# Optimization experiments

Measured on AMD Instinct MI355X. Metric: run time of the kernel, lower is better.

## Reference

```python
import jax, jax.numpy as jnp
import numpy as np

EPS = 1e-5

def _bn(x, g, b):
    # BatchNorm1d in training mode: stats over (batch, length) dims, biased var
    mean = jnp.mean(x, axis=(0, 2), keepdims=True)
    var = jnp.var(x, axis=(0, 2), keepdims=True)
    return (x - mean) * jax.lax.rsqrt(var + EPS) * g[None, :, None] + b[None, :, None]

def _conv1x1(x, w, b):
    # pointwise Conv1d: [B,C,T] x [O,C] -> [B,O,T]
    return jnp.einsum('bct,oc->bot', x, w) + b[None, :, None]

def setup_inputs() -> dict:
    key = jax.random.key(0)
    ks = jax.random.split(key, 4)
    B, C, T = 32, 1024, 2048
    x = jax.random.normal(ks[0], (B, C, T), dtype=jnp.float32)
    w1 = jax.random.normal(ks[1], (256, 1024), dtype=jnp.float32) * (1.0 / np.sqrt(1024))
    w2 = jax.random.normal(ks[2], (64, 256), dtype=jnp.float32) * (1.0 / np.sqrt(256))
    return {
        'x': x,
        'bn1_g': jnp.ones((1024,), jnp.float32), 'bn1_b': jnp.zeros((1024,), jnp.float32),
        'w1': w1, 'b1': jnp.zeros((256,), jnp.float32),
        'bn2_g': jnp.ones((256,), jnp.float32), 'bn2_b': jnp.zeros((256,), jnp.float32),
        'w2': w2, 'b2': jnp.zeros((64,), jnp.float32),
    }

def reference(x, bn1_g, bn1_b, w1, b1, bn2_g, bn2_b, w2, b2):
    # reduction layer: BN -> 1x1 conv -> ReLU (1024 -> 256)
    h = jax.nn.relu(_conv1x1(_bn(x, bn1_g, bn1_b), w1, b1))
    # out layer: BN -> 1x1 conv, no activation (256 -> 64)
    out = _conv1x1(_bn(h, bn2_g, bn2_b), w2, b2)
    o = out.shape[1]
    mu = out[:, : o // 2, :]
    logvar = out[:, o // 2 :, :]
    return (mu, logvar)
```

## Files before the change

kernel.cpp:

```cpp
#include <hip/hip_runtime.h>
#include <hip/hip_bf16.h>

#define B_  32
#define C1  1024
#define C2  256
#define T_  2048
#define EPSF 1e-5f
#define ROWP 40

typedef __attribute__((ext_vector_type(8))) short bf16x8;
typedef __attribute__((ext_vector_type(4))) float f32x4;

static __device__ __forceinline__ unsigned short f2bf(float f) {
    union { float f; unsigned u; } v; v.f = f;
    unsigned r = v.u + 0x7fffu + ((v.u >> 16) & 1u);
    return (unsigned short)(r >> 16);
}
static __device__ __forceinline__ float bf2f(unsigned short h) {
    union { unsigned u; float f; } v; v.u = ((unsigned)h) << 16;
    return v.f;
}

__global__ void k_stats1(const float* __restrict__ x,
                         const float* __restrict__ g1, const float* __restrict__ bb1,
                         float* __restrict__ scale1, float* __restrict__ shift1) {
    int c = blockIdx.x, tid = threadIdx.x;
    float s = 0.f, sq = 0.f;
    for (int b = 0; b < B_; ++b) {
        const float4* row = (const float4*)(x + (size_t)b * C1 * T_ + (size_t)c * T_);
        for (int i = tid; i < T_ / 4; i += 256) {
            float4 v = row[i];
            s  += v.x + v.y + v.z + v.w;
            sq += v.x * v.x + v.y * v.y + v.z * v.z + v.w * v.w;
        }
    }
    __shared__ float rs[256], rq[256];
    rs[tid] = s; rq[tid] = sq; __syncthreads();
    for (int off = 128; off > 0; off >>= 1) {
        if (tid < off) { rs[tid] += rs[tid + off]; rq[tid] += rq[tid + off]; }
        __syncthreads();
    }
    if (tid == 0) {
        float n = (float)(B_ * T_);
        float mean = rs[0] / n;
        float var  = rq[0] / n - mean * mean;
        float sc   = g1[c] * rsqrtf(var + EPSF);
        scale1[c] = sc;
        shift1[c] = bb1[c] - mean * sc;
    }
}

__global__ void k_fold1(const float* __restrict__ w1, const float* __restrict__ b1,
                        const float* __restrict__ scale1, const float* __restrict__ shift1,
                        unsigned short* __restrict__ w1e, float* __restrict__ b1e) {
    int o = blockIdx.x, tid = threadIdx.x;
    float4 w = ((const float4*)(w1 + (size_t)o * C1))[tid];
    int c = tid * 4;
    float p = w.x * shift1[c] + w.y * shift1[c + 1] + w.z * shift1[c + 2] + w.w * shift1[c + 3];
    uint2 pk;
    pk.x = (unsigned)f2bf(w.x * scale1[c])     | ((unsigned)f2bf(w.y * scale1[c + 1]) << 16);
    pk.y = (unsigned)f2bf(w.z * scale1[c + 2]) | ((unsigned)f2bf(w.w * scale1[c + 3]) << 16);
    *((uint2*)(w1e + (size_t)o * C1 + c)) = pk;
    __shared__ float rs[256];
    rs[tid] = p; __syncthreads();
    for (int off = 128; off > 0; off >>= 1) {
        if (tid < off) rs[tid] += rs[tid + off];
        __syncthreads();
    }
    if (tid == 0) b1e[o] = b1[o] + rs[0];
}

__global__ __launch_bounds__(256) void k_gemm1(const float* __restrict__ x,
        const unsigned short* __restrict__ w1e, const float* __restrict__ b1e,
        unsigned short* __restrict__ h) {
    __shared__ unsigned short sA[128 * ROWP];
    __shared__ unsigned short sB[128 * ROWP];
    int bm = blockIdx.x, bn = blockIdx.y, b = blockIdx.z;
    int tid = threadIdx.x;
    int wave = tid >> 6, lane = tid & 63;
    int wm = wave >> 1, wn = wave & 1;
    int l15 = lane & 15, q = lane >> 4;
    f32x4 acc[4][4] = {};
    const size_t xbase = (size_t)b * C1 * T_ + (size_t)bn * 128;

    for (int k0 = 0; k0 < C1; k0 += 32) {
        #pragma unroll
        for (int i = 0; i < 2; ++i) {
            int chunk = tid + i * 256;
            int row = chunk >> 2, cq = chunk & 3;
            uint4 v = *((const uint4*)(w1e + (size_t)(bm * 128 + row) * C1 + k0 + cq * 8));
            *((uint4*)&sA[row * ROWP + cq * 8]) = v;
        }
        #pragma unroll
        for (int i = 0; i < 2; ++i) {
            int task = tid + i * 256;
            int kp = task >> 5, tq = task & 31;
            const float* p0 = x + xbase + (size_t)(k0 + 2 * kp) * T_ + tq * 4;
            float4 r0 = *((const float4*)p0);
            float4 r1 = *((const float4*)(p0 + T_));
            int tl = tq * 4;
            *((unsigned*)&sB[(tl + 0) * ROWP + 2 * kp]) = (unsigned)f2bf(r0.x) | ((unsigned)f2bf(r1.x) << 16);
            *((unsigned*)&sB[(tl + 1) * ROWP + 2 * kp]) = (unsigned)f2bf(r0.y) | ((unsigned)f2bf(r1.y) << 16);
            *((unsigned*)&sB[(tl + 2) * ROWP + 2 * kp]) = (unsigned)f2bf(r0.z) | ((unsigned)f2bf(r1.z) << 16);
            *((unsigned*)&sB[(tl + 3) * ROWP + 2 * kp]) = (unsigned)f2bf(r0.w) | ((unsigned)f2bf(r1.w) << 16);
        }
        __syncthreads();
        bf16x8 af[4], bfr[4];
        #pragma unroll
        for (int mi = 0; mi < 4; ++mi)
            af[mi] = *((const bf16x8*)&sA[(wm * 64 + mi * 16 + l15) * ROWP + q * 8]);
        #pragma unroll
        for (int ni = 0; ni < 4; ++ni)
            bfr[ni] = *((const bf16x8*)&sB[(wn * 64 + ni * 16 + l15) * ROWP + q * 8]);
        #pragma unroll
        for (int mi = 0; mi < 4; ++mi)
            #pragma unroll
            for (int ni = 0; ni < 4; ++ni)
                acc[mi][ni] = __builtin_amdgcn_mfma_f32_16x16x32_bf16(af[mi], bfr[ni], acc[mi][ni], 0, 0, 0);
        __syncthreads();
    }
    int obase = bm * 128 + wm * 64;
    int tbase = bn * 128 + wn * 64;
    #pragma unroll
    for (int mi = 0; mi < 4; ++mi) {
        #pragma unroll
        for (int reg = 0; reg < 4; ++reg) {
            int o = obase + mi * 16 + q * 4 + reg;
            float bias = b1e[o];
            size_t hb = (size_t)b * C2 * T_ + (size_t)o * T_ + tbase;
            #pragma unroll
            for (int ni = 0; ni < 4; ++ni) {
                float v = acc[mi][ni][reg] + bias;
                v = v > 0.f ? v : 0.f;
                h[hb + ni * 16 + l15] = f2bf(v);
            }
        }
    }
}

__global__ void k_stats2(const unsigned short* __restrict__ h,
                         const float* __restrict__ g2, const float* __restrict__ bb2,
                         float* __restrict__ scale2, float* __restrict__ shift2) {
    int c = blockIdx.x, tid = threadIdx.x;
    float s = 0.f, sq = 0.f;
    for (int b = 0; b < B_; ++b) {
        const ushort4* row = (const ushort4*)(h + (size_t)b * C2 * T_ + (size_t)c * T_);
        for (int i = tid; i < T_ / 4; i += 256) {
            ushort4 v = row[i];
            float a0 = bf2f(v.x), a1 = bf2f(v.y), a2 = bf2f(v.z), a3 = bf2f(v.w);
            s  += a0 + a1 + a2 + a3;
            sq += a0 * a0 + a1 * a1 + a2 * a2 + a3 * a3;
        }
    }
    __shared__ float rs[256], rq[256];
    rs[tid] = s; rq[tid] = sq; __syncthreads();
    for (int off = 128; off > 0; off >>= 1) {
        if (tid < off) { rs[tid] += rs[tid + off]; rq[tid] += rq[tid + off]; }
        __syncthreads();
    }
    if (tid == 0) {
        float n = (float)(B_ * T_);
        float mean = rs[0] / n;
        float var  = rq[0] / n - mean * mean;
        float sc   = g2[c] * rsqrtf(var + EPSF);
        scale2[c] = sc;
        shift2[c] = bb2[c] - mean * sc;
    }
}

__global__ void k_fold2(const float* __restrict__ w2, const float* __restrict__ b2,
                        const float* __restrict__ scale2, const float* __restrict__ shift2,
                        unsigned short* __restrict__ w2e, float* __restrict__ b2e) {
    int o = blockIdx.x, tid = threadIdx.x;
    float w = w2[(size_t)o * C2 + tid];
    float p = w * shift2[tid];
    w2e[(size_t)o * C2 + tid] = f2bf(w * scale2[tid]);
    __shared__ float rs[256];
    rs[tid] = p; __syncthreads();
    for (int off = 128; off > 0; off >>= 1) {
        if (tid < off) rs[tid] += rs[tid + off];
        __syncthreads();
    }
    if (tid == 0) b2e[o] = b2[o] + rs[0];
}

__global__ __launch_bounds__(256) void k_gemm2(const unsigned short* __restrict__ h,
        const unsigned short* __restrict__ w2e, const float* __restrict__ b2e,
        float* __restrict__ out) {
    __shared__ unsigned short sA[64 * ROWP];
    __shared__ unsigned short sB[128 * ROWP];
    int bn = blockIdx.x, b = blockIdx.y;
    int tid = threadIdx.x;
    int wave = tid >> 6, lane = tid & 63;
    int l15 = lane & 15, q = lane >> 4;
    f32x4 acc[4][2] = {};
    const size_t hbase = (size_t)b * C2 * T_ + (size_t)bn * 128;

    for (int k0 = 0; k0 < C2; k0 += 32) {
        {
            int row = tid >> 2, cq = tid & 3;
            uint4 v = *((const uint4*)(w2e + (size_t)row * C2 + k0 + cq * 8));
            *((uint4*)&sA[row * ROWP + cq * 8]) = v;
        }
        #pragma unroll
        for (int i = 0; i < 2; ++i) {
            int task = tid + i * 256;
            int kp = task >> 5, tq = task & 31;
            const unsigned short* p0 = h + hbase + (size_t)(k0 + 2 * kp) * T_ + tq * 4;
            uint2 r0 = *((const uint2*)p0);
            uint2 r1 = *((const uint2*)(p0 + T_));
            unsigned a0 = r0.x & 0xffffu, a1 = r0.x >> 16, a2 = r0.y & 0xffffu, a3 = r0.y >> 16;
            unsigned c0 = r1.x & 0xffffu, c1 = r1.x >> 16, c2 = r1.y & 0xffffu, c3 = r1.y >> 16;
            int tl = tq * 4;
            *((unsigned*)&sB[(tl + 0) * ROWP + 2 * kp]) = a0 | (c0 << 16);
            *((unsigned*)&sB[(tl + 1) * ROWP + 2 * kp]) = a1 | (c1 << 16);
            *((unsigned*)&sB[(tl + 2) * ROWP + 2 * kp]) = a2 | (c2 << 16);
            *((unsigned*)&sB[(tl + 3) * ROWP + 2 * kp]) = a3 | (c3 << 16);
        }
        __syncthreads();
        bf16x8 af[4], bfr[2];
        #pragma unroll
        for (int mi = 0; mi < 4; ++mi)
            af[mi] = *((const bf16x8*)&sA[(mi * 16 + l15) * ROWP + q * 8]);
        #pragma unroll
        for (int ni = 0; ni < 2; ++ni)
            bfr[ni] = *((const bf16x8*)&sB[(wave * 32 + ni * 16 + l15) * ROWP + q * 8]);
        #pragma unroll
        for (int mi = 0; mi < 4; ++mi)
            #pragma unroll
            for (int ni = 0; ni < 2; ++ni)
                acc[mi][ni] = __builtin_amdgcn_mfma_f32_16x16x32_bf16(af[mi], bfr[ni], acc[mi][ni], 0, 0, 0);
        __syncthreads();
    }
    int tbase = bn * 128 + wave * 32;
    #pragma unroll
    for (int mi = 0; mi < 4; ++mi) {
        #pragma unroll
        for (int reg = 0; reg < 4; ++reg) {
            int o = mi * 16 + q * 4 + reg;
            float bias = b2e[o];
            size_t base = (o < 32)
                ? ((size_t)b * 32 * T_ + (size_t)o * T_)
                : (2097152u + (size_t)b * 32 * T_ + (size_t)(o - 32) * T_);
            #pragma unroll
            for (int ni = 0; ni < 2; ++ni) {
                int t = tbase + ni * 16 + l15;
                out[base + t] = acc[mi][ni][reg] + bias;
            }
        }
    }
}

extern "C" void kernel_launch(void* const* d_in, const int* in_sizes, int n_in,
                              void* d_out, int out_size, void* d_ws, size_t ws_size,
                              hipStream_t stream) {
    const float* x   = (const float*)d_in[0];
    const float* g1  = (const float*)d_in[1];
    const float* bb1 = (const float*)d_in[2];
    const float* w1  = (const float*)d_in[3];
    const float* b1  = (const float*)d_in[4];
    const float* g2  = (const float*)d_in[5];
    const float* bb2 = (const float*)d_in[6];
    const float* w2  = (const float*)d_in[7];
    const float* b2  = (const float*)d_in[8];
    float* out = (float*)d_out;

    char* ws = (char*)d_ws;
    float* scale1 = (float*)(ws + 0);
    float* shift1 = (float*)(ws + 4096);
    float* b1e    = (float*)(ws + 8192);
    float* scale2 = (float*)(ws + 9216);
    float* shift2 = (float*)(ws + 10240);
    float* b2e    = (float*)(ws + 11264);
    unsigned short* w1e = (unsigned short*)(ws + 12288);
    unsigned short* w2e = (unsigned short*)(ws + 12288 + 524288);
    unsigned short* h   = (unsigned short*)(ws + 573440);

    k_stats1<<<dim3(1024), dim3(256), 0, stream>>>(x, g1, bb1, scale1, shift1);
    k_fold1 <<<dim3(256),  dim3(256), 0, stream>>>(w1, b1, scale1, shift1, w1e, b1e);
    k_gemm1 <<<dim3(2, 16, 32), dim3(256), 0, stream>>>(x, w1e, b1e, h);
    k_stats2<<<dim3(256),  dim3(256), 0, stream>>>(h, g2, bb2, scale2, shift2);
    k_fold2 <<<dim3(64),   dim3(256), 0, stream>>>(w2, b2, scale2, shift2, w2e, b2e);
    k_gemm2 <<<dim3(16, 32), dim3(256), 0, stream>>>(h, w2e, b2e, out);
}
```

Measured before the change: 538.9 us.

## Transpose activations to channel-contiguous bf16 and load GEMM tiles directly to LDS

A new prep kernel reads x once. It computes the BN1 partial sums and also writes a bf16 copy of x transposed to [B,T,C]. Both GEMMs then load K-contiguous tiles with simple 16-byte loads, and GEMM1 uses global_load_lds to copy straight into shared memory. The intermediate h is also stored channel-contiguous, so stats2 becomes a coalesced partial reduction followed by a small finalize kernel. The aim is to avoid re-reading fp32 x for the statistics and to drop the per-element transpose and convert work inside the GEMM loops. In exchange it adds a 128 MB write and read of xT, and the unpadded 32-wide LDS rows may cause bank conflicts.

```diff
diff --git a/kernel.cpp b/kernel.cpp
--- a/kernel.cpp
+++ b/kernel.cpp
@@ -1,12 +1,11 @@
 #include <hip/hip_runtime.h>
-#include <hip/hip_bf16.h>
 
 #define B_  32
 #define C1  1024
 #define C2  256
 #define T_  2048
 #define EPSF 1e-5f
-#define ROWP 40
+#define CPAD 72
 
 typedef __attribute__((ext_vector_type(8))) short bf16x8;
 typedef __attribute__((ext_vector_type(4))) float f32x4;
@@ -20,34 +19,64 @@
     union { unsigned u; float f; } v; v.u = ((unsigned)h) << 16;
     return v.f;
 }
-
-__global__ void k_stats1(const float* __restrict__ x,
-                         const float* __restrict__ g1, const float* __restrict__ bb1,
-                         float* __restrict__ scale1, float* __restrict__ shift1) {
-    int c = blockIdx.x, tid = threadIdx.x;
-    float s = 0.f, sq = 0.f;
-    for (int b = 0; b < B_; ++b) {
-        const float4* row = (const float4*)(x + (size_t)b * C1 * T_ + (size_t)c * T_);
-        for (int i = tid; i < T_ / 4; i += 256) {
-            float4 v = row[i];
+static __device__ __forceinline__ void g2l16(const void* g, void* l) {
+    __builtin_amdgcn_global_load_lds(
+        (const __attribute__((address_space(1))) unsigned int*)g,
+        (__attribute__((address_space(3))) unsigned int*)l, 16, 0, 0);
+}
+
+__global__ __launch_bounds__(256) void k_prep(const float* __restrict__ x,
+        unsigned short* __restrict__ xT, float* __restrict__ psum, float* __restrict__ psq) {
+    __shared__ unsigned short tile[64 * CPAD];
+    __shared__ float red[256];
+    int ct = blockIdx.x, b = blockIdx.y, tid = threadIdx.x;
+    int c0 = ct * 64;
+    int cl = tid >> 2, t4 = tid & 3;
+    const float* xrow = x + (size_t)b * C1 * T_ + (size_t)(c0 + cl) * T_;
+    float s = 0.f, sq = 0.f;
+    for (int t0 = 0; t0 < T_; t0 += 64) {
+        #pragma unroll
+        for (int j = 0; j < 4; ++j) {
+            int tl = j * 16 + t4 * 4;
+            float4 v = *(const float4*)(xrow + t0 + tl);
             s  += v.x + v.y + v.z + v.w;
             sq += v.x * v.x + v.y * v.y + v.z * v.z + v.w * v.w;
-        }
-    }
-    __shared__ float rs[256], rq[256];
-    rs[tid] = s; rq[tid] = sq; __syncthreads();
-    for (int off = 128; off > 0; off >>= 1) {
-        if (tid < off) { rs[tid] += rs[tid + off]; rq[tid] += rq[tid + off]; }
-        __syncthreads();
-    }
-    if (tid == 0) {
-        float n = (float)(B_ * T_);
-        float mean = rs[0] / n;
-        float var  = rq[0] / n - mean * mean;
-        float sc   = g1[c] * rsqrtf(var + EPSF);
-        scale1[c] = sc;
-        shift1[c] = bb1[c] - mean * sc;
-    }
+            tile[(tl + 0) * CPAD + cl] = f2bf(v.x);
+            tile[(tl + 1) * CPAD + cl] = f2bf(v.y);
+            tile[(tl + 2) * CPAD + cl] = f2bf(v.z);
+            tile[(tl + 3) * CPAD + cl] = f2bf(v.w);
+        }
+        __syncthreads();
+        #pragma unroll
+        for (int j = 0; j < 2; ++j) {
+            int w = tid + j * 256;
+            int tl = w >> 3, cu = w & 7;
+            uint4 vv = *(const uint4*)&tile[tl * CPAD + cu * 8];
+            *(uint4*)&xT[((size_t)b * T_ + t0 + tl) * C1 + c0 + cu * 8] = vv;
+        }
+        __syncthreads();
+    }
+    red[tid] = s; __syncthreads();
+    if (tid < 64)
+        psum[(size_t)b * C1 + c0 + tid] = red[4*tid] + red[4*tid+1] + red[4*tid+2] + red[4*tid+3];
+    __syncthreads();
+    red[tid] = sq; __syncthreads();
+    if (tid < 64)
+        psq[(size_t)b * C1 + c0 + tid]  = red[4*tid] + red[4*tid+1] + red[4*tid+2] + red[4*tid+3];
+}
+
+__global__ void k_scales1(const float* __restrict__ psum, const float* __restrict__ psq,
+        const float* __restrict__ g, const float* __restrict__ bb,
+        float* __restrict__ scale, float* __restrict__ shift) {
+    int c = blockIdx.x * 256 + threadIdx.x;
+    float s = 0.f, sq = 0.f;
+    for (int b = 0; b < B_; ++b) { s += psum[b * C1 + c]; sq += psq[b * C1 + c]; }
+    float n = (float)(B_ * T_);
+    float mean = s / n;
+    float var  = sq / n - mean * mean;
+    float sc   = g[c] * rsqrtf(var + EPSF);
+    scale[c] = sc;
+    shift[c] = bb[c] - mean * sc;
 }
 
 __global__ void k_fold1(const float* __restrict__ w1, const float* __restrict__ b1,
@@ -70,48 +99,36 @@
     if (tid == 0) b1e[o] = b1[o] + rs[0];
 }
 
-__global__ __launch_bounds__(256) void k_gemm1(const float* __restrict__ x,
+__global__ __launch_bounds__(256) void k_gemm1(const unsigned short* __restrict__ xT,
         const unsigned short* __restrict__ w1e, const float* __restrict__ b1e,
-        unsigned short* __restrict__ h) {
-    __shared__ unsigned short sA[128 * ROWP];
-    __shared__ unsigned short sB[128 * ROWP];
+        unsigned short* __restrict__ hT) {
+    __shared__ unsigned short sA[128 * 32];
+    __shared__ unsigned short sB[128 * 32];
     int bm = blockIdx.x, bn = blockIdx.y, b = blockIdx.z;
     int tid = threadIdx.x;
     int wave = tid >> 6, lane = tid & 63;
     int wm = wave >> 1, wn = wave & 1;
     int l15 = lane & 15, q = lane >> 4;
     f32x4 acc[4][4] = {};
-    const size_t xbase = (size_t)b * C1 * T_ + (size_t)bn * 128;
+    const unsigned short* xblk = xT + ((size_t)b * T_ + (size_t)bn * 128) * C1;
+    const unsigned short* wblk = w1e + (size_t)(bm * 128) * C1;
 
     for (int k0 = 0; k0 < C1; k0 += 32) {
         #pragma unroll
         for (int i = 0; i < 2; ++i) {
-            int chunk = tid + i * 256;
-            int row = chunk >> 2, cq = chunk & 3;
-            uint4 v = *((const uint4*)(w1e + (size_t)(bm * 128 + row) * C1 + k0 + cq * 8));
-            *((uint4*)&sA[row * ROWP + cq * 8]) = v;
-        }
-        #pragma unroll
-        for (int i = 0; i < 2; ++i) {
-            int task = tid + i * 256;
-            int kp = task >> 5, tq = task & 31;
-            const float* p0 = x + xbase + (size_t)(k0 + 2 * kp) * T_ + tq * 4;
-            float4 r0 = *((const float4*)p0);
-            float4 r1 = *((const float4*)(p0 + T_));
-            int tl = tq * 4;
-            *((unsigned*)&sB[(tl + 0) * ROWP + 2 * kp]) = (unsigned)f2bf(r0.x) | ((unsigned)f2bf(r1.x) << 16);
-            *((unsigned*)&sB[(tl + 1) * ROWP + 2 * kp]) = (unsigned)f2bf(r0.y) | ((unsigned)f2bf(r1.y) << 16);
-            *((unsigned*)&sB[(tl + 2) * ROWP + 2 * kp]) = (unsigned)f2bf(r0.z) | ((unsigned)f2bf(r1.z) << 16);
-            *((unsigned*)&sB[(tl + 3) * ROWP + 2 * kp]) = (unsigned)f2bf(r0.w) | ((unsigned)f2bf(r1.w) << 16);
+            int idx = (wave * 2 + i) * 64 + lane;
+            int row = idx >> 2, cq = idx & 3;
+            g2l16(wblk + (size_t)row * C1 + k0 + cq * 8, &sA[(wave * 2 + i) * 512]);
+            g2l16(xblk + (size_t)row * C1 + k0 + cq * 8, &sB[(wave * 2 + i) * 512]);
         }
         __syncthreads();
         bf16x8 af[4], bfr[4];
         #pragma unroll
         for (int mi = 0; mi < 4; ++mi)
-            af[mi] = *((const bf16x8*)&sA[(wm * 64 + mi * 16 + l15) * ROWP + q * 8]);
+            af[mi] = *((const bf16x8*)&sA[(wm * 64 + mi * 16 + l15) * 32 + q * 8]);
         #pragma unroll
         for (int ni = 0; ni < 4; ++ni)
-            bfr[ni] = *((const bf16x8*)&sB[(wn * 64 + ni * 16 + l15) * ROWP + q * 8]);
+            bfr[ni] = *((const bf16x8*)&sB[(wn * 64 + ni * 16 + l15) * 32 + q * 8]);
         #pragma unroll
         for (int mi = 0; mi < 4; ++mi)
             #pragma unroll
@@ -123,49 +140,47 @@
     int tbase = bn * 128 + wn * 64;
     #pragma unroll
     for (int mi = 0; mi < 4; ++mi) {
-        #pragma unroll
-        for (int reg = 0; reg < 4; ++reg) {
-            int o = obase + mi * 16 + q * 4 + reg;
-            float bias = b1e[o];
-            size_t hb = (size_t)b * C2 * T_ + (size_t)o * T_ + tbase;
-            #pragma unroll
-            for (int ni = 0; ni < 4; ++ni) {
-                float v = acc[mi][ni][reg] + bias;
-                v = v > 0.f ? v : 0.f;
-                h[hb + ni * 16 + l15] = f2bf(v);
-            }
-        }
-    }
-}
-
-__global__ void k_stats2(const unsigned short* __restrict__ h,
-                         const float* __restrict__ g2, const float* __restrict__ bb2,
-                         float* __restrict__ scale2, float* __restrict__ shift2) {
-    int c = blockIdx.x, tid = threadIdx.x;
-    float s = 0.f, sq = 0.f;
-    for (int b = 0; b < B_; ++b) {
-        const ushort4* row = (const ushort4*)(h + (size_t)b * C2 * T_ + (size_t)c * T_);
-        for (int i = tid; i < T_ / 4; i += 256) {
-            ushort4 v = row[i];
-            float a0 = bf2f(v.x), a1 = bf2f(v.y), a2 = bf2f(v.z), a3 = bf2f(v.w);
-            s  += a0 + a1 + a2 + a3;
-            sq += a0 * a0 + a1 * a1 + a2 * a2 + a3 * a3;
-        }
-    }
-    __shared__ float rs[256], rq[256];
-    rs[tid] = s; rq[tid] = sq; __syncthreads();
-    for (int off = 128; off > 0; off >>= 1) {
-        if (tid < off) { rs[tid] += rs[tid + off]; rq[tid] += rq[tid + off]; }
-        __syncthreads();
-    }
-    if (tid == 0) {
-        float n = (float)(B_ * T_);
-        float mean = rs[0] / n;
-        float var  = rq[0] / n - mean * mean;
-        float sc   = g2[c] * rsqrtf(var + EPSF);
-        scale2[c] = sc;
-        shift2[c] = bb2[c] - mean * sc;
-    }
+        float4 bias = *(const float4*)&b1e[obase + mi * 16 + q * 4];
+        #pragma unroll
+        for (int ni = 0; ni < 4; ++ni) {
+            int t = tbase + ni * 16 + l15;
+            float v0 = fmaxf(acc[mi][ni][0] + bias.x, 0.f);
+            float v1 = fmaxf(acc[mi][ni][1] + bias.y, 0.f);
+            float v2 = fmaxf(acc[mi][ni][2] + bias.z, 0.f);
+            float v3 = fmaxf(acc[mi][ni][3] + bias.w, 0.f);
+            uint2 pk;
+            pk.x = (unsigned)f2bf(v0) | ((unsigned)f2bf(v1) << 16);
+            pk.y = (unsigned)f2bf(v2) | ((unsigned)f2bf(v3) << 16);
+            *(uint2*)&hT[((size_t)b * T_ + t) * C2 + obase + mi * 16 + q * 4] = pk;
+        }
+    }
+}
+
+__global__ __launch_bounds__(256) void k_stats2h(const unsigned short* __restrict__ hT,
+        float* __restrict__ p2s, float* __restrict__ p2q) {
+    int tid = threadIdx.x;
+    size_t r0 = (size_t)blockIdx.x * 128;
+    float s = 0.f, sq = 0.f;
+    for (int r = 0; r < 128; ++r) {
+        float v = bf2f(hT[(r0 + r) * C2 + tid]);
+        s += v; sq += v * v;
+    }
+    p2s[blockIdx.x * C2 + tid] = s;
+    p2q[blockIdx.x * C2 + tid] = sq;
+}
+
+__global__ void k_scales2(const float* __restrict__ p2s, const float* __restrict__ p2q,
+        const float* __restrict__ g, const float* __restrict__ bb,
+        float* __restrict__ scale, float* __restrict__ shift) {
+    int c = threadIdx.x;
+    float s = 0.f, sq = 0.f;
+    for (int i = 0; i < 512; ++i) { s += p2s[i * C2 + c]; sq += p2q[i * C2 + c]; }
+    float n = (float)(B_ * T_);
+    float mean = s / n;
+    float var  = sq / n - mean * mean;
+    float sc   = g[c] * rsqrtf(var + EPSF);
+    scale[c] = sc;
+    shift[c] = bb[c] - mean * sc;
 }
 
 __global__ void k_fold2(const float* __restrict__ w2, const float* __restrict__ b2,
@@ -184,47 +199,37 @@
     if (tid == 0) b2e[o] = b2[o] + rs[0];
 }
 
-__global__ __launch_bounds__(256) void k_gemm2(const unsigned short* __restrict__ h,
+__global__ __launch_bounds__(256) void k_gemm2(const unsigned short* __restrict__ hT,
         const unsigned short* __restrict__ w2e, const float* __restrict__ b2e,
         float* __restrict__ out) {
-    __shared__ unsigned short sA[64 * ROWP];
-    __shared__ unsigned short sB[128 * ROWP];
+    __shared__ unsigned short sA[64 * 32];
+    __shared__ unsigned short sB[128 * 32];
     int bn = blockIdx.x, b = blockIdx.y;
     int tid = threadIdx.x;
     int wave = tid >> 6, lane = tid & 63;
     int l15 = lane & 15, q = lane >> 4;
     f32x4 acc[4][2] = {};
-    const size_t hbase = (size_t)b * C2 * T_ + (size_t)bn * 128;
+    const unsigned short* hblk = hT + ((size_t)b * T_ + (size_t)bn * 128) * C2;
 
     for (int k0 = 0; k0 < C2; k0 += 32) {
         {
             int row = tid >> 2, cq = tid & 3;
-            uint4 v = *((const uint4*)(w2e + (size_t)row * C2 + k0 + cq * 8));
-            *((uint4*)&sA[row * ROWP + cq * 8]) = v;
+            *(uint4*)&sA[row * 32 + cq * 8] = *(const uint4*)(w2e + (size_t)row * C2 + k0 + cq * 8);
         }
         #pragma unroll
         for (int i = 0; i < 2; ++i) {
             int task = tid + i * 256;
-            int kp = task >> 5, tq = task & 31;
-            const unsigned short* p0 = h + hbase + (size_t)(k0 + 2 * kp) * T_ + tq * 4;
-            uint2 r0 = *((const uint2*)p0);
-            uint2 r1 = *((const uint2*)(p0 + T_));
-            unsigned a0 = r0.x & 0xffffu, a1 = r0.x >> 16, a2 = r0.y & 0xffffu, a3 = r0.y >> 16;
-            unsigned c0 = r1.x & 0xffffu, c1 = r1.x >> 16, c2 = r1.y & 0xffffu, c3 = r1.y >> 16;
-            int tl = tq * 4;
-            *((unsigned*)&sB[(tl + 0) * ROWP + 2 * kp]) = a0 | (c0 << 16);
-            *((unsigned*)&sB[(tl + 1) * ROWP + 2 * kp]) = a1 | (c1 << 16);
-            *((unsigned*)&sB[(tl + 2) * ROWP + 2 * kp]) = a2 | (c2 << 16);
-            *((unsigned*)&sB[(tl + 3) * ROWP + 2 * kp]) = a3 | (c3 << 16);
+            int row = task >> 2, cq = task & 3;
+            *(uint4*)&sB[row * 32 + cq * 8] = *(const uint4*)(hblk + (size_t)row * C2 + k0 + cq * 8);
         }
         __syncthreads();
         bf16x8 af[4], bfr[2];
         #pragma unroll
         for (int mi = 0; mi < 4; ++mi)
-            af[mi] = *((const bf16x8*)&sA[(mi * 16 + l15) * ROWP + q * 8]);
+            af[mi] = *((const bf16x8*)&sA[(mi * 16 + l15) * 32 + q * 8]);
         #pragma unroll
         for (int ni = 0; ni < 2; ++ni)
-            bfr[ni] = *((const bf16x8*)&sB[(wave * 32 + ni * 16 + l15) * ROWP + q * 8]);
+            bfr[ni] = *((const bf16x8*)&sB[(wave * 32 + ni * 16 + l15) * 32 + q * 8]);
         #pragma unroll
         for (int mi = 0; mi < 4; ++mi)
             #pragma unroll
@@ -269,17 +274,24 @@
     float* scale1 = (float*)(ws + 0);
     float* shift1 = (float*)(ws + 4096);
     float* b1e    = (float*)(ws + 8192);
-    float* scale2 = (float*)(ws + 9216);
-    float* shift2 = (float*)(ws + 10240);
-    float* b2e    = (float*)(ws + 11264);
-    unsigned short* w1e = (unsigned short*)(ws + 12288);
-    unsigned short* w2e = (unsigned short*)(ws + 12288 + 524288);
-    unsigned short* h   = (unsigned short*)(ws + 573440);
-
-    k_stats1<<<dim3(1024), dim3(256), 0, stream>>>(x, g1, bb1, scale1, shift1);
-    k_fold1 <<<dim3(256),  dim3(256), 0, stream>>>(w1, b1, scale1, shift1, w1e, b1e);
-    k_gemm1 <<<dim3(2, 16, 32), dim3(256), 0, stream>>>(x, w1e, b1e, h);
-    k_stats2<<<dim3(256),  dim3(256), 0, stream>>>(h, g2, bb2, scale2, shift2);
-    k_fold2 <<<dim3(64),   dim3(256), 0, stream>>>(w2, b2, scale2, shift2, w2e, b2e);
-    k_gemm2 <<<dim3(16, 32), dim3(256), 0, stream>>>(h, w2e, b2e, out);
-}
+    float* scale2 = (float*)(ws + 12288);
+    float* shift2 = (float*)(ws + 16384);
+    float* b2e    = (float*)(ws + 20480);
+    float* psum   = (float*)(ws + 24576);
+    float* psq    = (float*)(ws + 155648);
+    float* p2s    = (float*)(ws + 286720);
+    float* p2q    = (float*)(ws + 811008);
+    unsigned short* w1e = (unsigned short*)(ws + 1335296);
+    unsigned short* w2e = (unsigned short*)(ws + 1859584);
+    unsigned short* xT  = (unsigned short*)(ws + 1892352);
+    unsigned short* hT  = (unsigned short*)(ws + 1892352 + 134217728);
+
+    k_prep   <<<dim3(16, 32), dim3(256), 0, stream>>>(x, xT, psum, psq);
+    k_scales1<<<dim3(4),      dim3(256), 0, stream>>>(psum, psq, g1, bb1, scale1, shift1);
+    k_fold1  <<<dim3(256),    dim3(256), 0, stream>>>(w1, b1, scale1, shift1, w1e, b1e);
+    k_gemm1  <<<dim3(2, 16, 32), dim3(256), 0, stream>>>(xT, w1e, b1e, hT);
+    k_stats2h<<<dim3(512),    dim3(256), 0, stream>>>(hT, p2s, p2q);
+    k_scales2<<<dim3(1),      dim3(256), 0, stream>>>(p2s, p2q, g2, bb2, scale2, shift2);
+    k_fold2  <<<dim3(64),     dim3(256), 0, stream>>>(w2, b2, scale2, shift2, w2e, b2e);
+    k_gemm2  <<<dim3(16, 32), dim3(256), 0, stream>>>(hT, w2e, b2e, out);
+}
```

Result: no change. 538.1 us (-0.1%).
